# Kernel tuning notes

Measured on AMD Instinct MI355X. Metric: run time of the kernel, lower is better.

The kernel has to match this reference:

```python
import jax, jax.numpy as jnp
import numpy as np

L = 7  # window size (odd)
A = 0.1
B_COEF = 0.9


def mex_hat(d):
    grid = (np.mgrid[:d, :d] - d // 2) * 1.0
    eucl = (grid ** 2).sum(0) ** 0.5
    eucl /= d
    return eucl * np.exp(-eucl)


def setup_inputs() -> dict:
    key = jax.random.key(0)
    x = jax.random.normal(key, (16, 1, 512, 512), dtype=jnp.float32)
    kernel = jnp.asarray(mex_hat(L).reshape(-1), dtype=jnp.float32)  # [49], row-major like unfold
    return {"x": x, "kernel": kernel}


def reference(x, kernel):
    # x: [B,1,H,W], kernel: [L*L]
    # Extract zero-padded LxL patches, matching F.unfold(padding=L//2) ordering
    # (C=1, kernel positions row-major). patches: [B, L*L, H, W]
    patches = jax.lax.conv_general_dilated_patches(
        x, (L, L), (1, 1), 'SAME')
    average_term = jnp.exp(-patches.mean(axis=1, keepdims=True))  # [B,1,H,W]
    differential_term = jnp.sum(
        kernel[None, :, None, None] * jax.nn.relu(patches - x),
        axis=1, keepdims=True)  # [B,1,H,W]
    suppression = A * average_term + B_COEF * differential_term
    norm = jnp.sqrt(jnp.sum(suppression ** 2))
    suppression = suppression / norm
    mask = jnp.where(x > suppression, jnp.ones_like(x), jnp.zeros_like(x))
    return mask, average_term, differential_term
```

## Files before the change

### kernel.cpp

```cpp
#include <hip/hip_runtime.h>
#include <math.h>

#define HW 512
#define NB 16
#define TX 64
#define TY 32
#define LDSW 72
#define LDSH 38
#define N_PIX (NB * HW * HW)
#define NBLK (8 * 16 * NB)

__device__ __forceinline__ float sgpr_f(float v) {
    return __uint_as_float(__builtin_amdgcn_readfirstlane(__float_as_uint(v)));
}

__global__ __launch_bounds__(256, 8) void li_phase1(
    const float* __restrict__ x, const float* __restrict__ kw,
    float* __restrict__ out_ratio, float* __restrict__ out_avg,
    float* __restrict__ out_dif, float* __restrict__ partials)
{
    __shared__ float tile[LDSH * LDSW];
    __shared__ float wsum[4];

    const int tid = threadIdx.x;
    const int bx = blockIdx.x, by = blockIdx.y, b = blockIdx.z;
    const int x0 = bx * TX, y0 = by * TY;
    const float* xb = x + (size_t)b * (HW * HW);

    float w[49];
#pragma unroll
    for (int i = 0; i < 49; i++) w[i] = sgpr_f(kw[i]);

    for (int idx = tid; idx < LDSH * (LDSW / 4); idx += 256) {
        int r = idx / (LDSW / 4);
        int c4 = idx - r * (LDSW / 4);
        int gy = y0 - 3 + r;
        int gx = x0 - 4 + c4 * 4;
        float4 v = make_float4(0.f, 0.f, 0.f, 0.f);
        if ((unsigned)gy < HW && (unsigned)gx < HW)
            v = *(const float4*)(xb + gy * HW + gx);
        *(float4*)&tile[r * LDSW + c4 * 4] = v;
    }
    __syncthreads();

    const int tx  = tid & 63;
    const int ty0 = (tid >> 6) * 8;

    float cen[8];
#pragma unroll
    for (int p = 0; p < 8; p++)
        cen[p] = tile[(ty0 + p + 3) * LDSW + tx + 4];

    float dif[8]  = {0, 0, 0, 0, 0, 0, 0, 0};
    float bsum[8] = {0, 0, 0, 0, 0, 0, 0, 0};

#pragma unroll
    for (int r = 0; r < 14; r++) {
        float v[7];
#pragma unroll
        for (int dj = 0; dj < 7; dj++)
            v[dj] = tile[(ty0 + r) * LDSW + tx + 1 + dj];

        float rs = ((v[0] + v[1]) + (v[2] + v[3])) + ((v[4] + v[5]) + v[6]);
#pragma unroll
        for (int p = 0; p < 8; p++) {
            const int di = r - p;
            if (di >= 0 && di < 7) {
                bsum[p] += rs;
#pragma unroll
                for (int dj = 0; dj < 7; dj++)
                    dif[p] = fmaf(w[di * 7 + dj], fmaxf(v[dj] - cen[p], 0.f), dif[p]);
            }
        }
    }

    const size_t base = (size_t)b * (HW * HW) + (size_t)(y0 + ty0) * HW + x0 + tx;
    float ss = 0.f;
#pragma unroll
    for (int p = 0; p < 8; p++) {
        float avg = __expf(-bsum[p] * (1.0f / 49.0f));
        float d = dif[p];
        float sp = 0.1f * avg + 0.9f * d;
        size_t gi = base + (size_t)p * HW;
        __builtin_nontemporal_store(avg, out_avg + gi);
        __builtin_nontemporal_store(d,   out_dif + gi);
        out_ratio[gi] = cen[p] * __builtin_amdgcn_rcpf(sp);
        ss = fmaf(sp, sp, ss);
    }

#pragma unroll
    for (int off = 32; off > 0; off >>= 1)
        ss += __shfl_down(ss, off, 64);
    if ((tid & 63) == 0) wsum[tid >> 6] = ss;
    __syncthreads();
    if (tid == 0) {
        int flat = bx + 8 * (by + 16 * b);
        partials[flat] = (wsum[0] + wsum[1]) + (wsum[2] + wsum[3]);
    }
}

__global__ __launch_bounds__(256) void li_reduce(float* __restrict__ ws)
{
    __shared__ float wsum[4];
    const int tid = threadIdx.x;
    float s = 0.f;
#pragma unroll
    for (int i = 0; i < NBLK / 256; i++)
        s += ws[tid + i * 256];
#pragma unroll
    for (int off = 32; off > 0; off >>= 1)
        s += __shfl_down(s, off, 64);
    if ((tid & 63) == 0) wsum[tid >> 6] = s;
    __syncthreads();
    if (tid == 0)
        ws[NBLK] = 1.0f / sqrtf((wsum[0] + wsum[1]) + (wsum[2] + wsum[3]));
}

__global__ __launch_bounds__(256) void li_phase2(
    const float* __restrict__ ws, float* __restrict__ io)
{
    const int i = (blockIdx.x * 256 + threadIdx.x) * 4;
    const float inv = ws[NBLK];
    float4 r = *(const float4*)(io + i);
    float4 m;
    m.x = (r.x > inv) ? 1.f : 0.f;
    m.y = (r.y > inv) ? 1.f : 0.f;
    m.z = (r.z > inv) ? 1.f : 0.f;
    m.w = (r.w > inv) ? 1.f : 0.f;
    *(float4*)(io + i) = m;
}

extern "C" void kernel_launch(void* const* d_in, const int* in_sizes, int n_in,
                              void* d_out, int out_size, void* d_ws, size_t ws_size,
                              hipStream_t stream) {
    const float* x  = (const float*)d_in[0];
    const float* kw = (const float*)d_in[1];
    float* out   = (float*)d_out;
    float* ratio = out;
    float* avg   = out + N_PIX;
    float* dif   = out + 2 * (size_t)N_PIX;
    float* ws    = (float*)d_ws;

    dim3 g(HW / TX, HW / TY, NB);
    li_phase1<<<g, 256, 0, stream>>>(x, kw, ratio, avg, dif, ws);
    li_reduce<<<1, 256, 0, stream>>>(ws);
    li_phase2<<<N_PIX / 1024, 256, 0, stream>>>(ws, ratio);
}
```

Baseline: 97.24 us.

## Enlarge phase1 tiles, skip zero center tap, fuse reduction into mask kernel

Doubles the phase1 tile height to 64 rows, so each thread computes 16 outputs instead of 8 and the halo overhead per output drops. The center tap is skipped because relu(x - x) is always zero. The separate single-block reduction kernel is removed: every phase2 block now re-reduces the 1024 partials itself and handles 4096 elements, which saves one launch at the cost of redundant reduction work per block. The larger tile and doubled per-thread register state lower occupancy, reflected in the launch bound going from 8 to 4 blocks.

```diff
diff --git a/kernel.cpp b/kernel.cpp
--- a/kernel.cpp
+++ b/kernel.cpp
@@ -4,17 +4,17 @@
 #define HW 512
 #define NB 16
 #define TX 64
-#define TY 32
+#define TY 64
 #define LDSW 72
-#define LDSH 38
+#define LDSH 70
 #define N_PIX (NB * HW * HW)
-#define NBLK (8 * 16 * NB)
+#define NBLK (8 * 8 * NB)
 
 __device__ __forceinline__ float sgpr_f(float v) {
     return __uint_as_float(__builtin_amdgcn_readfirstlane(__float_as_uint(v)));
 }
 
-__global__ __launch_bounds__(256, 8) void li_phase1(
+__global__ __launch_bounds__(256, 4) void li_phase1(
     const float* __restrict__ x, const float* __restrict__ kw,
     float* __restrict__ out_ratio, float* __restrict__ out_avg,
     float* __restrict__ out_dif, float* __restrict__ partials)
@@ -44,18 +44,19 @@
     __syncthreads();
 
     const int tx  = tid & 63;
-    const int ty0 = (tid >> 6) * 8;
+    const int ty0 = (tid >> 6) * 16;
 
-    float cen[8];
+    float cen[16];
 #pragma unroll
-    for (int p = 0; p < 8; p++)
+    for (int p = 0; p < 16; p++)
         cen[p] = tile[(ty0 + p + 3) * LDSW + tx + 4];
 
-    float dif[8]  = {0, 0, 0, 0, 0, 0, 0, 0};
-    float bsum[8] = {0, 0, 0, 0, 0, 0, 0, 0};
+    float dif[16], bsum[16];
+#pragma unroll
+    for (int p = 0; p < 16; p++) { dif[p] = 0.f; bsum[p] = 0.f; }
 
 #pragma unroll
-    for (int r = 0; r < 14; r++) {
+    for (int r = 0; r < 22; r++) {
         float v[7];
 #pragma unroll
         for (int dj = 0; dj < 7; dj++)
@@ -63,13 +64,15 @@
 
         float rs = ((v[0] + v[1]) + (v[2] + v[3])) + ((v[4] + v[5]) + v[6]);
 #pragma unroll
-        for (int p = 0; p < 8; p++) {
+        for (int p = 0; p < 16; p++) {
             const int di = r - p;
             if (di >= 0 && di < 7) {
                 bsum[p] += rs;
 #pragma unroll
-                for (int dj = 0; dj < 7; dj++)
+                for (int dj = 0; dj < 7; dj++) {
+                    if (di == 3 && dj == 3) continue;
                     dif[p] = fmaf(w[di * 7 + dj], fmaxf(v[dj] - cen[p], 0.f), dif[p]);
+                }
             }
         }
     }
@@ -77,7 +80,7 @@
     const size_t base = (size_t)b * (HW * HW) + (size_t)(y0 + ty0) * HW + x0 + tx;
     float ss = 0.f;
 #pragma unroll
-    for (int p = 0; p < 8; p++) {
+    for (int p = 0; p < 16; p++) {
         float avg = __expf(-bsum[p] * (1.0f / 49.0f));
         float d = dif[p];
         float sp = 0.1f * avg + 0.9f * d;
@@ -93,41 +96,43 @@
         ss += __shfl_down(ss, off, 64);
     if ((tid & 63) == 0) wsum[tid >> 6] = ss;
     __syncthreads();
-    if (tid == 0) {
-        int flat = bx + 8 * (by + 16 * b);
-        partials[flat] = (wsum[0] + wsum[1]) + (wsum[2] + wsum[3]);
-    }
+    if (tid == 0)
+        partials[bx + 8 * (by + 8 * b)] = (wsum[0] + wsum[1]) + (wsum[2] + wsum[3]);
 }
 
-__global__ __launch_bounds__(256) void li_reduce(float* __restrict__ ws)
+__global__ __launch_bounds__(256) void li_phase2(
+    const float* __restrict__ partials, float* __restrict__ io)
 {
     __shared__ float wsum[4];
+    __shared__ float s_inv;
     const int tid = threadIdx.x;
+
     float s = 0.f;
 #pragma unroll
     for (int i = 0; i < NBLK / 256; i++)
-        s += ws[tid + i * 256];
+        s += partials[tid + i * 256];
 #pragma unroll
     for (int off = 32; off > 0; off >>= 1)
         s += __shfl_down(s, off, 64);
     if ((tid & 63) == 0) wsum[tid >> 6] = s;
     __syncthreads();
     if (tid == 0)
-        ws[NBLK] = 1.0f / sqrtf((wsum[0] + wsum[1]) + (wsum[2] + wsum[3]));
-}
+        s_inv = 1.0f / sqrtf((wsum[0] + wsum[1]) + (wsum[2] + wsum[3]));
+    __syncthreads();
 
-__global__ __launch_bounds__(256) void li_phase2(
-    const float* __restrict__ ws, float* __restrict__ io)
-{
-    const int i = (blockIdx.x * 256 + threadIdx.x) * 4;
-    const float inv = ws[NBLK];
-    float4 r = *(const float4*)(io + i);
-    float4 m;
-    m.x = (r.x > inv) ? 1.f : 0.f;
-    m.y = (r.y > inv) ? 1.f : 0.f;
-    m.z = (r.z > inv) ? 1.f : 0.f;
-    m.w = (r.w > inv) ? 1.f : 0.f;
-    *(float4*)(io + i) = m;
+    const float inv = s_inv;
+    const int base = blockIdx.x * 4096 + tid * 4;
+#pragma unroll
+    for (int k = 0; k < 4; k++) {
+        const int i = base + k * 1024;
+        float4 r = *(const float4*)(io + i);
+        float4 m;
+        m.x = (r.x > inv) ? 1.f : 0.f;
+        m.y = (r.y > inv) ? 1.f : 0.f;
+        m.z = (r.z > inv) ? 1.f : 0.f;
+        m.w = (r.w > inv) ? 1.f : 0.f;
+        *(float4*)(io + i) = m;
+    }
 }
 
 extern "C" void kernel_launch(void* const* d_in, const int* in_sizes, int n_in,
@@ -143,6 +148,5 @@
 
     dim3 g(HW / TX, HW / TY, NB);
     li_phase1<<<g, 256, 0, stream>>>(x, kw, ratio, avg, dif, ws);
-    li_reduce<<<1, 256, 0, stream>>>(ws);
-    li_phase2<<<N_PIX / 1024, 256, 0, stream>>>(ws, ratio);
+    li_phase2<<<N_PIX / 4096, 256, 0, stream>>>(ws, ratio);
 }
```

New measurement: 98.05 us. About the same (+0.8%).
